# Kernel optimization log

Measured on AMD Instinct MI355X. Metric: run time of the kernel, lower is better.

## Reference

```python
import jax, jax.numpy as jnp
import numpy as np

IN_CH, D, K = 256, 128, 512

def setup_inputs() -> dict:
    key = jax.random.key(0)
    k1, k2, k3, k4 = jax.random.split(key, 4)
    x = jax.random.normal(k1, (16, IN_CH, 64, 64), dtype=jnp.float32)
    W = jax.random.normal(k2, (D, IN_CH), dtype=jnp.float32) * (1.0 / np.sqrt(IN_CH))
    b = jax.random.normal(k3, (D,), dtype=jnp.float32) * 0.01
    prototypes = jax.random.normal(k4, (K, D), dtype=jnp.float32) * 0.02
    gamma = jnp.asarray(1.0, dtype=jnp.float32)
    return {"x": x, "W": W, "b": b, "prototypes": prototypes, "gamma": gamma}

def reference(x, W, b, prototypes, gamma):
    n, c, h, w = x.shape
    # 1x1 conv projection: [n,c,h,w] -> [n,h,w,d]
    q = jnp.einsum('nchw,dc->nhwd', x, W) + b
    q_flat = q.reshape(n * h * w, -1)                      # [T, d]
    q_norm2 = jnp.sum(q_flat * q_flat, axis=1, keepdims=True)   # [T, 1]
    p_norm2 = jnp.sum(prototypes * prototypes, axis=1)[None, :] # [1, K]
    dist2 = q_norm2 + p_norm2 - 2.0 * (q_flat @ prototypes.T)   # [T, K]
    weights = jax.nn.softmax(-jnp.abs(gamma) * dist2, axis=1)
    return weights.reshape(n, h, w, -1).transpose(0, 3, 1, 2)   # [n, K, h, w]
```

## Files before the change

kernel.cpp:

```cpp
#include <hip/hip_runtime.h>

#define HW 4096
#define NCH 256
#define DIM 128
#define NPROTO 512

typedef __attribute__((ext_vector_type(4))) float f32x4;
typedef __attribute__((ext_vector_type(8))) short s16x8;

__device__ __forceinline__ unsigned short f2bf(float f) {
  union { float f; unsigned u; } v; v.f = f;
  unsigned r = v.u + 0x7fffu + ((v.u >> 16) & 1u);
  return (unsigned short)(r >> 16);
}
__device__ __forceinline__ float bf2f(unsigned short h) {
  union { unsigned u; float f; } v; v.u = ((unsigned)h) << 16;
  return v.f;
}

__global__ __launch_bounds__(256) void prep_kernel(const float* __restrict__ P,
                                                   unsigned short* __restrict__ Pr,
                                                   float* __restrict__ pn2) {
  const int tid = threadIdx.x;
  const int n  = blockIdx.x * 64 + (tid >> 2);
  const int qt = tid & 3;
  const float* row = P + n * DIM + qt * 32;
  unsigned short* dst = Pr + ((size_t)qt * NPROTO + n) * 32;
  float ssq = 0.f;
#pragma unroll
  for (int u = 0; u < 8; ++u) {
    f32x4 v = *(const f32x4*)(row + 4 * u);
    ssq += v.x * v.x + v.y * v.y + v.z * v.z + v.w * v.w;
    dst[4 * u + 0] = f2bf(v.x);
    dst[4 * u + 1] = f2bf(v.y);
    dst[4 * u + 2] = f2bf(v.z);
    dst[4 * u + 3] = f2bf(v.w);
  }
  ssq += __shfl_xor(ssq, 1);
  ssq += __shfl_xor(ssq, 2);
  if (qt == 0) pn2[n] = ssq;
}

__global__ __launch_bounds__(512) void proj_kernel(const float* __restrict__ x,
                                                   const float* __restrict__ Wm,
                                                   const float* __restrict__ bias,
                                                   unsigned short* __restrict__ qbf) {
  __shared__ __align__(16) unsigned short x_s[128 * 72];
  __shared__ __align__(16) unsigned short w_s[128 * 72];
  const int tid  = threadIdx.x;
  const int p0   = blockIdx.x * 128;
  const int nimg = p0 >> 12;
  const int hw0  = p0 & 4095;
  const float* xbase = x + (size_t)nimg * NCH * HW + hw0;
  const int wave = tid >> 6, lane = tid & 63;
  const int l15 = lane & 15, l4 = lane >> 4;

  f32x4 acc[8];
#pragma unroll
  for (int j = 0; j < 8; ++j)
#pragma unroll
    for (int r = 0; r < 4; ++r) acc[j][r] = 0.f;

  for (int c0 = 0; c0 < NCH; c0 += 64) {
    {
      const int f = tid & 31, cl = tid >> 5;
#pragma unroll
      for (int r = 0; r < 4; ++r) {
        const int cc = cl + 16 * r;
        f32x4 v = *(const f32x4*)(xbase + (size_t)(c0 + cc) * HW + 4 * f);
        x_s[(4 * f + 0) * 72 + cc] = f2bf(v.x);
        x_s[(4 * f + 1) * 72 + cc] = f2bf(v.y);
        x_s[(4 * f + 2) * 72 + cc] = f2bf(v.z);
        x_s[(4 * f + 3) * 72 + cc] = f2bf(v.w);
      }
      const int f2 = tid & 15, dl = tid >> 4;
#pragma unroll
      for (int r = 0; r < 4; ++r) {
        const int d = dl + 32 * r;
        f32x4 v = *(const f32x4*)(Wm + d * NCH + c0 + 4 * f2);
        unsigned short* w = &w_s[d * 72 + 4 * f2];
        w[0] = f2bf(v.x); w[1] = f2bf(v.y); w[2] = f2bf(v.z); w[3] = f2bf(v.w);
      }
    }
    __syncthreads();
#pragma unroll
    for (int kc = 0; kc < 64; kc += 32) {
      s16x8 a = *(const s16x8*)&x_s[(16 * wave + l15) * 72 + kc + 8 * l4];
#pragma unroll
      for (int j = 0; j < 8; ++j) {
        s16x8 b = *(const s16x8*)&w_s[(16 * j + l15) * 72 + kc + 8 * l4];
        acc[j] = __builtin_amdgcn_mfma_f32_16x16x32_bf16(a, b, acc[j], 0, 0, 0);
      }
    }
    __syncthreads();
  }
  const int mb = 16 * wave + 4 * l4;
#pragma unroll
  for (int j = 0; j < 8; ++j) {
    const int d = 16 * j + l15;
    const float bv = bias[d];
#pragma unroll
    for (int r = 0; r < 4; ++r)
      qbf[(size_t)(p0 + mb + r) * DIM + d] = f2bf(acc[j][r] + bv);
  }
}

__global__ __launch_bounds__(512) void attn_kernel(const unsigned short* __restrict__ qbf,
                                                   const unsigned short* __restrict__ Pr,
                                                   const float* __restrict__ pn2,
                                                   const float* __restrict__ gptr,
                                                   float* __restrict__ out) {
  __shared__ __align__(16) char smem[58368];
  unsigned short* q_s = (unsigned short*)smem;
  unsigned short* P_s = (unsigned short*)(smem + 17408);
  unsigned short* w_s = (unsigned short*)smem;
  float* red  = (float*)(smem + 36864);
  float* rmx  = (float*)(smem + 36864 + 2048);
  float* rinv = (float*)(smem + 36864 + 2048 + 256);

  const int tid  = threadIdx.x;
  const int p0   = blockIdx.x * 64;
  const int nimg = p0 >> 12;
  const int hw0  = p0 & 4095;
  const int wave = tid >> 6, lane = tid & 63;
  const int l15 = lane & 15, l4 = lane >> 4;
  const float g = fabsf(gptr[0]);

  {
    const int r = tid >> 3, c8 = tid & 7;
#pragma unroll
    for (int it = 0; it < 2; ++it) {
      const int col = c8 + 8 * it;
      s16x8 v = *(const s16x8*)(qbf + (size_t)(p0 + r) * DIM + 8 * col);
      *(s16x8*)&q_s[r * 136 + 8 * col] = v;
    }
  }

  f32x4 acc[4][4];
#pragma unroll
  for (int i = 0; i < 4; ++i)
#pragma unroll
    for (int j = 0; j < 4; ++j)
#pragma unroll
      for (int r = 0; r < 4; ++r) acc[i][j][r] = 0.f;

  for (int ch = 0; ch < 4; ++ch) {
    if (ch) __syncthreads();
    {
      const unsigned short* src = Pr + ((size_t)ch * NPROTO + tid) * 32;
      unsigned short* dst = &P_s[tid * 40];
#pragma unroll
      for (int u = 0; u < 4; ++u)
        *(s16x8*)(dst + 8 * u) = *(const s16x8*)(src + 8 * u);
    }
    __syncthreads();
    const int dk = ch * 32;
    s16x8 afr[4];
#pragma unroll
    for (int i = 0; i < 4; ++i)
      afr[i] = *(const s16x8*)&q_s[(16 * i + l15) * 136 + dk + 8 * l4];
#pragma unroll
    for (int j = 0; j < 4; ++j) {
      s16x8 bfr = *(const s16x8*)&P_s[(64 * wave + 16 * j + l15) * 40 + 8 * l4];
#pragma unroll
      for (int i = 0; i < 4; ++i)
        acc[i][j] = __builtin_amdgcn_mfma_f32_16x16x32_bf16(afr[i], bfr, acc[i][j], 0, 0, 0);
    }
  }
  __syncthreads();

  float pnv[4];
#pragma unroll
  for (int j = 0; j < 4; ++j) pnv[j] = pn2[64 * wave + 16 * j + l15];

#pragma unroll
  for (int i = 0; i < 4; ++i)
#pragma unroll
    for (int r = 0; r < 4; ++r) {
      float m = -1e30f;
#pragma unroll
      for (int j = 0; j < 4; ++j) {
        float lv = g * (2.f * acc[i][j][r] - pnv[j]);
        acc[i][j][r] = lv;
        m = fmaxf(m, lv);
      }
#pragma unroll
      for (int s = 1; s < 16; s <<= 1) m = fmaxf(m, __shfl_xor(m, s));
      if (l15 == 0) red[wave * 64 + 16 * i + 4 * l4 + r] = m;
    }
  __syncthreads();
  if (tid < 64) {
    float M = red[tid];
#pragma unroll
    for (int w = 1; w < 8; ++w) M = fmaxf(M, red[w * 64 + tid]);
    rmx[tid] = M;
  }
  __syncthreads();

#pragma unroll
  for (int i = 0; i < 4; ++i)
#pragma unroll
    for (int r = 0; r < 4; ++r) {
      const float M = rmx[16 * i + 4 * l4 + r];
      float s = 0.f;
#pragma unroll
      for (int j = 0; j < 4; ++j) {
        float e = __expf(acc[i][j][r] - M);
        acc[i][j][r] = e;
        s += e;
      }
#pragma unroll
      for (int t = 1; t < 16; t <<= 1) s += __shfl_xor(s, t);
      if (l15 == 0) red[wave * 64 + 16 * i + 4 * l4 + r] = s;
    }
  __syncthreads();
  if (tid < 64) {
    float S = 0.f;
#pragma unroll
    for (int w = 0; w < 8; ++w) S += red[w * 64 + tid];
    rinv[tid] = 1.f / S;
  }
  __syncthreads();

  float inv[4][4];
#pragma unroll
  for (int i = 0; i < 4; ++i)
#pragma unroll
    for (int r = 0; r < 4; ++r) inv[i][r] = rinv[16 * i + 4 * l4 + r];

  const size_t outbase = (size_t)nimg * NPROTO * HW + hw0;
#pragma unroll
  for (int half = 0; half < 2; ++half) {
    if ((wave >> 2) == half) {
      const int wl = wave & 3;
#pragma unroll
      for (int i = 0; i < 4; ++i)
#pragma unroll
        for (int j = 0; j < 4; ++j) {
          const int nl = 64 * wl + 16 * j + l15;
#pragma unroll
          for (int r = 0; r < 4; ++r)
            w_s[nl * 72 + 16 * i + 4 * l4 + r] = f2bf(acc[i][j][r] * inv[i][r]);
        }
    }
    __syncthreads();
    {
      const int f4 = tid & 15, kl = tid >> 4;
#pragma unroll
      for (int it = 0; it < 8; ++it) {
        const int kloc = kl + 32 * it;
        const unsigned short* src = &w_s[kloc * 72 + 4 * f4];
        f32x4 o;
        o.x = bf2f(src[0]); o.y = bf2f(src[1]);
        o.z = bf2f(src[2]); o.w = bf2f(src[3]);
        *(f32x4*)(out + outbase + (size_t)(half * 256 + kloc) * HW + 4 * f4) = o;
      }
    }
    __syncthreads();
  }
}

extern "C" void kernel_launch(void* const* d_in, const int* in_sizes, int n_in,
                              void* d_out, int out_size, void* d_ws, size_t ws_size,
                              hipStream_t stream) {
  const float* x     = (const float*)d_in[0];
  const float* Wm    = (const float*)d_in[1];
  const float* bias  = (const float*)d_in[2];
  const float* prot  = (const float*)d_in[3];
  const float* gamma = (const float*)d_in[4];
  float* out = (float*)d_out;

  unsigned short* q_ws  = (unsigned short*)d_ws;
  unsigned short* P_ws  = (unsigned short*)((char*)d_ws + 16777216);
  float*          pn2_w = (float*)((char*)d_ws + 16777216 + 131072);

  prep_kernel<<<8, 256, 0, stream>>>(prot, P_ws, pn2_w);
  proj_kernel<<<512, 512, 0, stream>>>(x, Wm, bias, q_ws);
  attn_kernel<<<1024, 512, 0, stream>>>(q_ws, P_ws, pn2_w, gamma, out);
}
```

Baseline: 225.6 us.

## Pre-convert W to bf16, double-buffer x in proj, drop LDS staging in attn

The prep kernel now also converts W to a chunked bf16 layout, so proj_kernel reads W fragments straight from global/L2 instead of staging them through LDS. proj_kernel double-buffers 32-channel x slices in LDS with one sync per chunk and declares occupancy 2. attn_kernel reads prototype fragments directly from global memory instead of staging them in LDS. It also writes fp32 output straight from registers rather than round-tripping through a bf16 LDS tile, which also removes that intermediate bf16 rounding. The aim is fewer barriers and less LDS traffic, at the cost of redundant global loads per wave and less contiguous output stores.

Result: slower. 248.3 us (+10.1%).

```diff
diff --git a/kernel.cpp b/kernel.cpp
--- a/kernel.cpp
+++ b/kernel.cpp
@@ -7,46 +7,63 @@
 
 typedef __attribute__((ext_vector_type(4))) float f32x4;
 typedef __attribute__((ext_vector_type(8))) short s16x8;
+typedef __attribute__((ext_vector_type(4))) unsigned u32x4;
 
 __device__ __forceinline__ unsigned short f2bf(float f) {
   union { float f; unsigned u; } v; v.f = f;
   unsigned r = v.u + 0x7fffu + ((v.u >> 16) & 1u);
   return (unsigned short)(r >> 16);
 }
-__device__ __forceinline__ float bf2f(unsigned short h) {
-  union { unsigned u; float f; } v; v.u = ((unsigned)h) << 16;
-  return v.f;
-}
 
 __global__ __launch_bounds__(256) void prep_kernel(const float* __restrict__ P,
+                                                   const float* __restrict__ Wm,
                                                    unsigned short* __restrict__ Pr,
+                                                   unsigned short* __restrict__ Wr,
                                                    float* __restrict__ pn2) {
   const int tid = threadIdx.x;
-  const int n  = blockIdx.x * 64 + (tid >> 2);
-  const int qt = tid & 3;
-  const float* row = P + n * DIM + qt * 32;
-  unsigned short* dst = Pr + ((size_t)qt * NPROTO + n) * 32;
-  float ssq = 0.f;
-#pragma unroll
-  for (int u = 0; u < 8; ++u) {
-    f32x4 v = *(const f32x4*)(row + 4 * u);
-    ssq += v.x * v.x + v.y * v.y + v.z * v.z + v.w * v.w;
-    dst[4 * u + 0] = f2bf(v.x);
-    dst[4 * u + 1] = f2bf(v.y);
-    dst[4 * u + 2] = f2bf(v.z);
-    dst[4 * u + 3] = f2bf(v.w);
-  }
-  ssq += __shfl_xor(ssq, 1);
-  ssq += __shfl_xor(ssq, 2);
-  if (qt == 0) pn2[n] = ssq;
-}
-
-__global__ __launch_bounds__(512) void proj_kernel(const float* __restrict__ x,
-                                                   const float* __restrict__ Wm,
-                                                   const float* __restrict__ bias,
-                                                   unsigned short* __restrict__ qbf) {
-  __shared__ __align__(16) unsigned short x_s[128 * 72];
-  __shared__ __align__(16) unsigned short w_s[128 * 72];
+  if (blockIdx.x < 8) {
+    const int n  = blockIdx.x * 64 + (tid >> 2);
+    const int qt = tid & 3;
+    const float* row = P + n * DIM + qt * 32;
+    unsigned short* dst = Pr + ((size_t)qt * NPROTO + n) * 32;
+    float ssq = 0.f;
+#pragma unroll
+    for (int u = 0; u < 8; ++u) {
+      f32x4 v = *(const f32x4*)(row + 4 * u);
+      ssq += v.x * v.x + v.y * v.y + v.z * v.z + v.w * v.w;
+      dst[4 * u + 0] = f2bf(v.x);
+      dst[4 * u + 1] = f2bf(v.y);
+      dst[4 * u + 2] = f2bf(v.z);
+      dst[4 * u + 3] = f2bf(v.w);
+    }
+    ssq += __shfl_xor(ssq, 1);
+    ssq += __shfl_xor(ssq, 2);
+    if (qt == 0) pn2[n] = ssq;
+  } else {
+#pragma unroll
+    for (int it = 0; it < 2; ++it) {
+      const int p  = (blockIdx.x - 8) * 256 + tid + 512 * it;
+      const int d  = p >> 3;
+      const int ch = p & 7;
+      const float* src = Wm + d * NCH + 32 * ch;
+      unsigned short* dst = Wr + ((size_t)ch * DIM + d) * 32;
+#pragma unroll
+      for (int u = 0; u < 8; ++u) {
+        f32x4 v = *(const f32x4*)(src + 4 * u);
+        dst[4 * u + 0] = f2bf(v.x);
+        dst[4 * u + 1] = f2bf(v.y);
+        dst[4 * u + 2] = f2bf(v.z);
+        dst[4 * u + 3] = f2bf(v.w);
+      }
+    }
+  }
+}
+
+__global__ __launch_bounds__(512, 2) void proj_kernel(const float* __restrict__ x,
+                                                      const unsigned short* __restrict__ Wr,
+                                                      const float* __restrict__ bias,
+                                                      unsigned short* __restrict__ qbf) {
+  __shared__ __align__(16) unsigned short x_s[2][128 * 40];
   const int tid  = threadIdx.x;
   const int p0   = blockIdx.x * 128;
   const int nimg = p0 >> 12;
@@ -54,6 +71,8 @@
   const float* xbase = x + (size_t)nimg * NCH * HW + hw0;
   const int wave = tid >> 6, lane = tid & 63;
   const int l15 = lane & 15, l4 = lane >> 4;
+  const int pix = tid & 127;
+  const int qq  = tid >> 7;
 
   f32x4 acc[8];
 #pragma unroll
@@ -61,39 +80,42 @@
 #pragma unroll
     for (int r = 0; r < 4; ++r) acc[j][r] = 0.f;
 
-  for (int c0 = 0; c0 < NCH; c0 += 64) {
-    {
-      const int f = tid & 31, cl = tid >> 5;
-#pragma unroll
-      for (int r = 0; r < 4; ++r) {
-        const int cc = cl + 16 * r;
-        f32x4 v = *(const f32x4*)(xbase + (size_t)(c0 + cc) * HW + 4 * f);
-        x_s[(4 * f + 0) * 72 + cc] = f2bf(v.x);
-        x_s[(4 * f + 1) * 72 + cc] = f2bf(v.y);
-        x_s[(4 * f + 2) * 72 + cc] = f2bf(v.z);
-        x_s[(4 * f + 3) * 72 + cc] = f2bf(v.w);
-      }
-      const int f2 = tid & 15, dl = tid >> 4;
-#pragma unroll
-      for (int r = 0; r < 4; ++r) {
-        const int d = dl + 32 * r;
-        f32x4 v = *(const f32x4*)(Wm + d * NCH + c0 + 4 * f2);
-        unsigned short* w = &w_s[d * 72 + 4 * f2];
-        w[0] = f2bf(v.x); w[1] = f2bf(v.y); w[2] = f2bf(v.z); w[3] = f2bf(v.w);
-      }
+  {
+    const float* src = xbase + (size_t)(8 * qq) * HW + pix;
+    u32x4 vv;
+#pragma unroll
+    for (int jj = 0; jj < 4; ++jj) {
+      float f0 = src[(size_t)(2 * jj) * HW];
+      float f1 = src[(size_t)(2 * jj + 1) * HW];
+      vv[jj] = (unsigned)f2bf(f0) | ((unsigned)f2bf(f1) << 16);
+    }
+    *(u32x4*)&x_s[0][pix * 40 + 8 * qq] = vv;
+  }
+  __syncthreads();
+
+  const int m = 16 * wave + l15;
+  for (int ch = 0; ch < 8; ++ch) {
+    if (ch < 7) {
+      const float* src = xbase + (size_t)(32 * (ch + 1) + 8 * qq) * HW + pix;
+      u32x4 vv;
+#pragma unroll
+      for (int jj = 0; jj < 4; ++jj) {
+        float f0 = src[(size_t)(2 * jj) * HW];
+        float f1 = src[(size_t)(2 * jj + 1) * HW];
+        vv[jj] = (unsigned)f2bf(f0) | ((unsigned)f2bf(f1) << 16);
+      }
+      *(u32x4*)&x_s[(ch + 1) & 1][pix * 40 + 8 * qq] = vv;
+    }
+    s16x8 a = *(const s16x8*)&x_s[ch & 1][m * 40 + 8 * l4];
+    const unsigned short* wbase = Wr + ((size_t)ch * DIM + l15) * 32 + 8 * l4;
+#pragma unroll
+    for (int j = 0; j < 8; ++j) {
+      s16x8 b = *(const s16x8*)(wbase + (size_t)(16 * j) * 32);
+      acc[j] = __builtin_amdgcn_mfma_f32_16x16x32_bf16(a, b, acc[j], 0, 0, 0);
     }
     __syncthreads();
-#pragma unroll
-    for (int kc = 0; kc < 64; kc += 32) {
-      s16x8 a = *(const s16x8*)&x_s[(16 * wave + l15) * 72 + kc + 8 * l4];
-#pragma unroll
-      for (int j = 0; j < 8; ++j) {
-        s16x8 b = *(const s16x8*)&w_s[(16 * j + l15) * 72 + kc + 8 * l4];
-        acc[j] = __builtin_amdgcn_mfma_f32_16x16x32_bf16(a, b, acc[j], 0, 0, 0);
-      }
-    }
-    __syncthreads();
-  }
+  }
+
   const int mb = 16 * wave + 4 * l4;
 #pragma unroll
   for (int j = 0; j < 8; ++j) {
@@ -110,13 +132,10 @@
                                                    const float* __restrict__ pn2,
                                                    const float* __restrict__ gptr,
                                                    float* __restrict__ out) {
-  __shared__ __align__(16) char smem[58368];
-  unsigned short* q_s = (unsigned short*)smem;
-  unsigned short* P_s = (unsigned short*)(smem + 17408);
-  unsigned short* w_s = (unsigned short*)smem;
-  float* red  = (float*)(smem + 36864);
-  float* rmx  = (float*)(smem + 36864 + 2048);
-  float* rinv = (float*)(smem + 36864 + 2048 + 256);
+  __shared__ __align__(16) unsigned short q_s[64 * 136];
+  float* red  = (float*)q_s;
+  float* rmx  = (float*)q_s + 512;
+  float* rinv = (float*)q_s + 576;
 
   const int tid  = threadIdx.x;
   const int p0   = blockIdx.x * 64;
@@ -135,6 +154,7 @@
       *(s16x8*)&q_s[r * 136 + 8 * col] = v;
     }
   }
+  __syncthreads();
 
   f32x4 acc[4][4];
 #pragma unroll
@@ -144,24 +164,16 @@
 #pragma unroll
       for (int r = 0; r < 4; ++r) acc[i][j][r] = 0.f;
 
+#pragma unroll
   for (int ch = 0; ch < 4; ++ch) {
-    if (ch) __syncthreads();
-    {
-      const unsigned short* src = Pr + ((size_t)ch * NPROTO + tid) * 32;
-      unsigned short* dst = &P_s[tid * 40];
-#pragma unroll
-      for (int u = 0; u < 4; ++u)
-        *(s16x8*)(dst + 8 * u) = *(const s16x8*)(src + 8 * u);
-    }
-    __syncthreads();
-    const int dk = ch * 32;
     s16x8 afr[4];
 #pragma unroll
     for (int i = 0; i < 4; ++i)
-      afr[i] = *(const s16x8*)&q_s[(16 * i + l15) * 136 + dk + 8 * l4];
+      afr[i] = *(const s16x8*)&q_s[(16 * i + l15) * 136 + 32 * ch + 8 * l4];
+    const unsigned short* pb = Pr + ((size_t)ch * NPROTO + 64 * wave + l15) * 32 + 8 * l4;
 #pragma unroll
     for (int j = 0; j < 4; ++j) {
-      s16x8 bfr = *(const s16x8*)&P_s[(64 * wave + 16 * j + l15) * 40 + 8 * l4];
+      s16x8 bfr = *(const s16x8*)(pb + (size_t)(16 * j) * 32);
 #pragma unroll
       for (int i = 0; i < 4; ++i)
         acc[i][j] = __builtin_amdgcn_mfma_f32_16x16x32_bf16(afr[i], bfr, acc[i][j], 0, 0, 0);
@@ -230,33 +242,15 @@
 
   const size_t outbase = (size_t)nimg * NPROTO * HW + hw0;
 #pragma unroll
-  for (int half = 0; half < 2; ++half) {
-    if ((wave >> 2) == half) {
-      const int wl = wave & 3;
-#pragma unroll
-      for (int i = 0; i < 4; ++i)
-#pragma unroll
-        for (int j = 0; j < 4; ++j) {
-          const int nl = 64 * wl + 16 * j + l15;
-#pragma unroll
-          for (int r = 0; r < 4; ++r)
-            w_s[nl * 72 + 16 * i + 4 * l4 + r] = f2bf(acc[i][j][r] * inv[i][r]);
-        }
-    }
-    __syncthreads();
-    {
-      const int f4 = tid & 15, kl = tid >> 4;
-#pragma unroll
-      for (int it = 0; it < 8; ++it) {
-        const int kloc = kl + 32 * it;
-        const unsigned short* src = &w_s[kloc * 72 + 4 * f4];
-        f32x4 o;
-        o.x = bf2f(src[0]); o.y = bf2f(src[1]);
-        o.z = bf2f(src[2]); o.w = bf2f(src[3]);
-        *(f32x4*)(out + outbase + (size_t)(half * 256 + kloc) * HW + 4 * f4) = o;
-      }
-    }
-    __syncthreads();
+  for (int j = 0; j < 4; ++j) {
+    float* op = out + outbase + (size_t)(64 * wave + 16 * j + l15) * HW + 4 * l4;
+#pragma unroll
+    for (int i = 0; i < 4; ++i) {
+      f32x4 o;
+#pragma unroll
+      for (int r = 0; r < 4; ++r) o[r] = acc[i][j][r] * inv[i][r];
+      *(f32x4*)(op + 16 * i) = o;
+    }
   }
 }
 
@@ -272,9 +266,10 @@
 
   unsigned short* q_ws  = (unsigned short*)d_ws;
   unsigned short* P_ws  = (unsigned short*)((char*)d_ws + 16777216);
-  float*          pn2_w = (float*)((char*)d_ws + 16777216 + 131072);
-
-  prep_kernel<<<8, 256, 0, stream>>>(prot, P_ws, pn2_w);
-  proj_kernel<<<512, 512, 0, stream>>>(x, Wm, bias, q_ws);
+  unsigned short* W_ws  = (unsigned short*)((char*)d_ws + 16777216 + 131072);
+  float*          pn2_w = (float*)((char*)d_ws + 16777216 + 131072 + 65536);
+
+  prep_kernel<<<10, 256, 0, stream>>>(prot, Wm, P_ws, W_ws, pn2_w);
+  proj_kernel<<<512, 512, 0, stream>>>(x, W_ws, bias, q_ws);
   attn_kernel<<<1024, 512, 0, stream>>>(q_ws, P_ws, pn2_w, gamma, out);
 }
```
